# Performance work log

Measured on AMD Instinct MI355X. Metric: run time of the kernel, lower is better.

## Reference

```python
import jax, jax.numpy as jnp
import numpy as np

B, L, D, H, FF = 2, 2048, 2048, 16, 8192
DH = D // H
NEG = -1e9


def setup_inputs() -> dict:
    key = jax.random.key(0)
    ks = jax.random.split(key, 9)
    x = jax.random.normal(ks[0], (B, L, D), dtype=jnp.float32)
    # additive causal mask, broadcastable to [B, H, L, L]
    causal = jnp.triu(jnp.full((L, L), NEG, dtype=jnp.float32), k=1)
    mask = causal[None, None, :, :]
    s = 1.0 / np.sqrt(D)
    Wq = jax.random.normal(ks[1], (D, D), dtype=jnp.float32) * s
    Wk = jax.random.normal(ks[2], (D, D), dtype=jnp.float32) * s
    Wv = jax.random.normal(ks[3], (D, D), dtype=jnp.float32) * s
    Wo = jax.random.normal(ks[4], (D, D), dtype=jnp.float32) * s
    W_up = jax.random.normal(ks[5], (FF, D), dtype=jnp.float32) * s
    b_up = jnp.zeros((FF,), dtype=jnp.float32)
    W_down = jax.random.normal(ks[6], (D, FF), dtype=jnp.float32) * (1.0 / np.sqrt(FF))
    return {"x": x, "mask": mask, "Wq": Wq, "Wk": Wk, "Wv": Wv, "Wo": Wo,
            "W_up": W_up, "b_up": b_up, "W_down": W_down}


def reference(x, mask, Wq, Wk, Wv, Wo, W_up, b_up, W_down):
    b, l, d = x.shape
    # projections (torch Linear: y = x @ W.T); reshape to [B, H, L, DH]
    q = (x @ Wq.T).reshape(b, l, H, DH).transpose(0, 2, 1, 3)
    k = (x @ Wk.T).reshape(b, l, H, DH).transpose(0, 2, 1, 3)
    v = (x @ Wv.T).reshape(b, l, H, DH).transpose(0, 2, 1, 3)
    # NOTE: original module applies NO 1/sqrt(d_head) scaling
    scores = jnp.einsum('bhqd,bhkd->bhqk', q, k) + mask
    attn = jax.nn.softmax(scores, axis=-1)
    out = jnp.einsum('bhqk,bhkd->bhqd', attn, v)
    out = out.transpose(0, 2, 1, 3).reshape(b, l, d)
    x = x + out @ Wo.T
    h = jax.nn.relu(x @ W_up.T + b_up)
    return x + h @ W_down.T
```

## Files before the change

kernel.cpp:

```cpp
#include <hip/hip_runtime.h>
#include <stdint.h>

typedef _Float16 f16;
typedef __attribute__((ext_vector_type(8))) _Float16 f16x8;
typedef __attribute__((ext_vector_type(4))) _Float16 f16x4;
typedef __attribute__((ext_vector_type(4))) float f32x4;
typedef __attribute__((ext_vector_type(16))) float f32x16;

__device__ __forceinline__ void gload16(void* lds, const void* gc) {
  void* g = const_cast<void*>(gc);
  __builtin_amdgcn_global_load_lds((__attribute__((address_space(1))) void*)g,
                                   (__attribute__((address_space(3))) void*)lds,
                                   16, 0, 0);
}

__global__ __launch_bounds__(256) void k_cast(const float* __restrict__ in,
                                              f16* __restrict__ out, int n4) {
  int stride = gridDim.x * blockDim.x;
  for (int i = blockIdx.x * blockDim.x + threadIdx.x; i < n4; i += stride) {
    float4 v = ((const float4*)in)[i];
    f16x4 o;
    o[0] = (f16)v.x; o[1] = (f16)v.y; o[2] = (f16)v.z; o[3] = (f16)v.w;
    ((f16x4*)out)[i] = o;
  }
}

__global__ __launch_bounds__(256) void k_cast4(const float* __restrict__ s0, const float* __restrict__ s1,
                                               const float* __restrict__ s2, const float* __restrict__ s3,
                                               f16* __restrict__ d0, f16* __restrict__ d1,
                                               f16* __restrict__ d2, f16* __restrict__ d3, int n4) {
  const int which = blockIdx.y;
  const float* in = which == 0 ? s0 : which == 1 ? s1 : which == 2 ? s2 : s3;
  f16* out = which == 0 ? d0 : which == 1 ? d1 : which == 2 ? d2 : d3;
  int stride = gridDim.x * blockDim.x;
  for (int i = blockIdx.x * blockDim.x + threadIdx.x; i < n4; i += stride) {
    float4 v = ((const float4*)in)[i];
    f16x4 o;
    o[0] = (f16)v.x; o[1] = (f16)v.y; o[2] = (f16)v.z; o[3] = (f16)v.w;
    ((f16x4*)out)[i] = o;
  }
}

__global__ __launch_bounds__(256) void k_cast2w(const float* __restrict__ s0, const float* __restrict__ s1,
                                                f16* __restrict__ d0, f16* __restrict__ d1, int n4) {
  const int which = blockIdx.y;
  const float* in = which == 0 ? s0 : s1;
  f16* out = which == 0 ? d0 : d1;
  int stride = gridDim.x * blockDim.x;
  for (int i = blockIdx.x * blockDim.x + threadIdx.x; i < n4; i += stride) {
    float4 v = ((const float4*)in)[i];
    f16x4 o;
    o[0] = (f16)v.x; o[1] = (f16)v.y; o[2] = (f16)v.z; o[3] = (f16)v.w;
    ((f16x4*)out)[i] = o;
  }
}

__global__ __launch_bounds__(256) void k_transpose_v(const f16* __restrict__ vp,
                                                     f16* __restrict__ vt) {
  __shared__ __attribute__((aligned(16))) f16 tile[64][66];
  const int lt = blockIdx.x, dt = blockIdx.y, bh = blockIdx.z;
  const int t = threadIdx.x;
  const int r = t >> 3, c = 8 * (t & 7);
  const f16* src = vp + ((size_t)bh * 2048 + lt * 64) * 128 + dt * 64;
#pragma unroll
  for (int i = 0; i < 2; ++i) {
    union { f16x8 v; unsigned u[4]; } uu;
    uu.v = *(const f16x8*)&src[(size_t)(i * 32 + r) * 128 + c];
#pragma unroll
    for (int j = 0; j < 4; ++j)
      *(unsigned*)&tile[i * 32 + r][c + 2 * j] = uu.u[j];
  }
  __syncthreads();
  f16* dst = vt + ((size_t)bh * 128 + dt * 64) * 2048 + lt * 64;
#pragma unroll
  for (int i = 0; i < 2; ++i) {
    const int dr = i * 32 + r;
    f16x8 o;
#pragma unroll
    for (int e = 0; e < 8; ++e) o[e] = tile[c + e][dr];
    *(f16x8*)&dst[(size_t)dr * 2048 + c] = o;
  }
}

__global__ __launch_bounds__(256) void k_fuseout(const f16* __restrict__ x1b,
                                                 const float* __restrict__ p0,
                                                 const float* __restrict__ p1,
                                                 float* __restrict__ out, int n4) {
  int stride = gridDim.x * blockDim.x;
  for (int i = blockIdx.x * blockDim.x + threadIdx.x; i < n4; i += stride) {
    float4 a = ((const float4*)p0)[i];
    float4 b = ((const float4*)p1)[i];
    f16x4 xb = ((const f16x4*)x1b)[i];
    float4 o;
    o.x = (float)xb[0] + a.x + b.x;
    o.y = (float)xb[1] + a.y + b.y;
    o.z = (float)xb[2] + a.z + b.z;
    o.w = (float)xb[3] + a.w + b.w;
    ((float4*)out)[i] = o;
  }
}

template <int EPI, int SPLITOUT, int BK>
__global__ __launch_bounds__(256, 4) void gemm_nt(const f16* __restrict__ A,
                                                  const f16* __restrict__ B,
                                                  int Kit, int ld, int N,
                                                  const float* __restrict__ res,
                                                  const float* __restrict__ bias,
                                                  float* __restrict__ outf,
                                                  float* __restrict__ outf2,
                                                  f16* __restrict__ outb,
                                                  f16* __restrict__ outb_lo,
                                                  f16* __restrict__ outv) {
  constexpr int TSZ = 128 * BK;
  constexpr int CH  = 2048;
  constexpr int RPC = CH / BK;
  constexpr int NCH = 128 / RPC;
  constexpr int CW  = BK / 8;
  __shared__ __attribute__((aligned(16))) f16 As[TSZ];
  __shared__ __attribute__((aligned(16))) f16 Bs[TSZ];
  const int t = threadIdx.x;
  const int l = t & 63;
  const int w = t >> 6;
  const int wr = w >> 1, wc = w & 1;

  const int nwg = gridDim.x * gridDim.y;
  const int id = blockIdx.y * gridDim.x + blockIdx.x;
  const int sw = (id & 7) * (nwg >> 3) + (id >> 3);
  const int bn = sw % gridDim.x;
  const int bm = sw / gridDim.x;
  const int k0 = blockIdx.z * Kit;

  f32x4 acc[4][4] = {};

  const size_t aoff = (size_t)bm * 128 * ld + k0;
  const size_t boff = (size_t)bn * 128 * ld + k0;

  const int sr = t / CW;
  const int sc = 8 * (t % CW);
  const int lbase = w * 512;

  const int lr = l & 15, lq = l >> 4;
  const int nk = Kit / BK;
  for (int kt = 0; kt < nk; ++kt) {
    const size_t gbase = (size_t)kt * BK + (size_t)sr * ld + sc;
#pragma unroll
    for (int j = 0; j < NCH; ++j) {
      gload16(As + j * CH + lbase, A + aoff + (size_t)j * RPC * ld + gbase);
      gload16(Bs + j * CH + lbase, B + boff + (size_t)j * RPC * ld + gbase);
    }
    __syncthreads();
#pragma unroll
    for (int kk = 0; kk < BK / 32; ++kk) {
      f16x8 af[4], bfr[4];
#pragma unroll
      for (int m = 0; m < 4; ++m)
        af[m] = *(const f16x8*)&As[(wr * 64 + m * 16 + lr) * BK + kk * 32 + 8 * lq];
#pragma unroll
      for (int n = 0; n < 4; ++n)
        bfr[n] = *(const f16x8*)&Bs[(wc * 64 + n * 16 + lr) * BK + kk * 32 + 8 * lq];
#pragma unroll
      for (int m = 0; m < 4; ++m)
#pragma unroll
        for (int n = 0; n < 4; ++n)
          acc[m][n] = __builtin_amdgcn_mfma_f32_16x16x32_f16(af[m], bfr[n], acc[m][n], 0, 0, 0);
    }
    __syncthreads();
  }

  const size_t QKS = (size_t)8 << 20;
#pragma unroll
  for (int m = 0; m < 4; ++m) {
#pragma unroll
    for (int r = 0; r < 4; ++r) {
      const int grow = bm * 128 + wr * 64 + m * 16 + lq * 4 + r;
#pragma unroll
      for (int n = 0; n < 4; ++n) {
        const int gcol = bn * 128 + wc * 64 + n * 16 + lr;
        const float v = acc[m][n][r];
        if constexpr (EPI == 0) {
          const int which = gcol >> 11;
          const int hcol = gcol & 2047;
          const int bb = grow >> 11, ll = grow & 2047;
          const int hh = hcol >> 7, dh = hcol & 127;
          const size_t idx = ((size_t)((bb * 16 + hh) * 2048 + ll) << 7) + dh;
          const f16 hv = (f16)v;
          if (which == 2) {
            outv[idx] = hv;
          } else {
            outb[which * QKS + idx] = hv;
            if constexpr (SPLITOUT) outb_lo[which * QKS + idx] = (f16)(v - (float)hv);
          }
        } else if constexpr (EPI == 1) {
          const size_t idx = (size_t)grow * N + gcol;
          outb[idx] = (f16)(res[idx] + v);
        } else if constexpr (EPI == 2) {
          const size_t idx = (size_t)grow * N + gcol;
          outb[idx] = (f16)fmaxf(v + bias[gcol], 0.f);
        } else {
          const size_t idx = (size_t)grow * N + gcol;
          (blockIdx.z ? outf2 : outf)[idx] = v;
        }
      }
    }
  }
}

__global__ __launch_bounds__(256) void k_attn(const f16* __restrict__ q_hi,
                                              const f16* __restrict__ q_lo,
                                              const f16* __restrict__ k_hi,
                                              const f16* __restrict__ k_lo,
                                              const f16* __restrict__ vtp,
                                              f16* __restrict__ op) {
  __shared__ __attribute__((aligned(16))) f16 Ks_hi[64 * 128];
  __shared__ __attribute__((aligned(16))) f16 Ks_lo[64 * 128];
  __shared__ __attribute__((aligned(16))) f16 Vs[128 * 64];
  __shared__ __attribute__((aligned(16))) f16 Ps[4][32 * 64];
  const int t = threadIdx.x, l = t & 63, w = t >> 6;
  const int flat = (int)blockIdx.x;
  const int s_ = flat >> 5;
  const int bh = flat & 31;
  const int qb = (s_ < 8) ? (15 - s_) : (s_ - 8);
  const int q0 = qb * 128;
  const int lh = l >> 5, lm = l & 31;
  const int wrow0 = q0 + 32 * w;
  const int myrow = wrow0 + lm;

  const f16* qhp = q_hi + (size_t)bh * 2048 * 128;
  const f16* qlp = q_lo + (size_t)bh * 2048 * 128;
  const f16* khp = k_hi + (size_t)bh * 2048 * 128;
  const f16* klp = k_lo + (size_t)bh * 2048 * 128;
  const f16* vhp = vtp + (size_t)bh * 128 * 2048;

  const int krow = t >> 4, kg = t & 15;
  const int vrow = t >> 3, vg = t & 7;

  f16x8 aqh[8], aql[8];
#pragma unroll
  for (int c = 0; c < 8; ++c) {
    const size_t qi = (size_t)myrow * 128 + c * 16 + 8 * lh;
    aqh[c] = *(const f16x8*)&qhp[qi];
    aql[c] = *(const f16x8*)&qlp[qi];
  }

  f32x16 acc[4] = {};
  float mr[16], sr[16];
#pragma unroll
  for (int j = 0; j < 16; ++j) { mr[j] = -1e30f; sr[j] = 0.f; }

  const int ntile = 2 * qb + 2;
  for (int kt = 0; kt < ntile; ++kt) {
    f16x8 tkh[4], tkl[4], tv[4];
#pragma unroll
    for (int i = 0; i < 4; ++i) {
      const size_t ki = (size_t)(kt * 64 + i * 16 + krow) * 128 + 8 * kg;
      tkh[i] = *(const f16x8*)&khp[ki];
      tkl[i] = *(const f16x8*)&klp[ki];
      tv[i] = *(const f16x8*)&vhp[(size_t)(i * 32 + vrow) * 2048 + kt * 64 + 8 * vg];
    }
    __syncthreads();
#pragma unroll
    for (int i = 0; i < 4; ++i) {
      const int kr = i * 16 + krow;
      const int g = kg ^ (kr & 7);
      *(f16x8*)&Ks_hi[kr * 128 + 8 * g] = tkh[i];
      *(f16x8*)&Ks_lo[kr * 128 + 8 * g] = tkl[i];
      const int vr = i * 32 + vrow;
      const int gv = vg ^ (vr & 7);
      *(f16x8*)&Vs[vr * 64 + 8 * gv] = tv[i];
    }
    __syncthreads();

    if (kt * 64 >= wrow0 + 32) continue;

    f32x16 s0, s1;
    __builtin_amdgcn_s_setprio(1);
    {
      f32x16 zh = {}, zl = {};
#pragma unroll
      for (int c = 0; c < 8; ++c) {
        const int g = (2 * c + lh) ^ (lm & 7);
        const f16x8 bh_ = *(const f16x8*)&Ks_hi[lm * 128 + 8 * g];
        const f16x8 bl_ = *(const f16x8*)&Ks_lo[lm * 128 + 8 * g];
        zh = __builtin_amdgcn_mfma_f32_32x32x16_f16(aqh[c], bh_, zh, 0, 0, 0);
        zl = __builtin_amdgcn_mfma_f32_32x32x16_f16(aql[c], bh_, zl, 0, 0, 0);
        zl = __builtin_amdgcn_mfma_f32_32x32x16_f16(aqh[c], bl_, zl, 0, 0, 0);
      }
      s0 = zh + zl;
    }
    {
      f32x16 zh = {}, zl = {};
#pragma unroll
      for (int c = 0; c < 8; ++c) {
        const int g = (2 * c + lh) ^ (lm & 7);
        const f16x8 bh_ = *(const f16x8*)&Ks_hi[(32 + lm) * 128 + 8 * g];
        const f16x8 bl_ = *(const f16x8*)&Ks_lo[(32 + lm) * 128 + 8 * g];
        zh = __builtin_amdgcn_mfma_f32_32x32x16_f16(aqh[c], bh_, zh, 0, 0, 0);
        zl = __builtin_amdgcn_mfma_f32_32x32x16_f16(aql[c], bh_, zl, 0, 0, 0);
        zl = __builtin_amdgcn_mfma_f32_32x32x16_f16(aqh[c], bl_, zl, 0, 0, 0);
      }
      s1 = zh + zl;
    }
    __builtin_amdgcn_s_setprio(0);

    if (kt * 64 + 63 > wrow0) {
#pragma unroll
      for (int j = 0; j < 16; ++j) {
        const int rg = wrow0 + (j & 3) + 8 * (j >> 2) + 4 * lh;
        if (kt * 64 + lm > rg) s0[j] = -1e30f;
        if (kt * 64 + 32 + lm > rg) s1[j] = -1e30f;
      }
    }

    float mx[16];
#pragma unroll
    for (int j = 0; j < 16; ++j) {
      float m = fmaxf(s0[j], s1[j]);
#pragma unroll
      for (int off = 1; off < 32; off <<= 1)
        m = fmaxf(m, __shfl_xor(m, off));
      mx[j] = m;
    }
    bool grew = false;
#pragma unroll
    for (int j = 0; j < 16; ++j) grew = grew || (mx[j] > mr[j] + 8.f);
    if (__any(grew)) {
#pragma unroll
      for (int j = 0; j < 16; ++j) {
        const float mnew = fmaxf(mr[j], mx[j]);
        const float sc = __expf(mr[j] - mnew);
        mr[j] = mnew;
        sr[j] *= sc;
#pragma unroll
        for (int ct = 0; ct < 4; ++ct) acc[ct][j] *= sc;
      }
    }
#pragma unroll
    for (int j = 0; j < 16; ++j) {
      const int rjl = (j & 3) + 8 * (j >> 2) + 4 * lh;
      const float p0v = __expf(s0[j] - mr[j]);
      const float p1v = __expf(s1[j] - mr[j]);
      float ts = p0v + p1v;
#pragma unroll
      for (int off = 1; off < 32; off <<= 1)
        ts += __shfl_xor(ts, off);
      sr[j] += ts;
      const int g0 = (lm >> 3) ^ (rjl & 7);
      Ps[w][rjl * 64 + 8 * g0 + (lm & 7)] = (f16)p0v;
      const int g1 = (4 + (lm >> 3)) ^ (rjl & 7);
      Ps[w][rjl * 64 + 8 * g1 + (lm & 7)] = (f16)p1v;
    }

    f16x8 pf[4];
#pragma unroll
    for (int kk = 0; kk < 4; ++kk) {
      const int g = (2 * kk + lh) ^ (lm & 7);
      pf[kk] = *(const f16x8*)&Ps[w][lm * 64 + 8 * g];
    }
    __builtin_amdgcn_s_setprio(1);
#pragma unroll
    for (int ct = 0; ct < 4; ++ct) {
      const int dcol = ct * 32 + lm;
#pragma unroll
      for (int kk = 0; kk < 4; ++kk) {
        const int gv = (2 * kk + lh) ^ (dcol & 7);
        const f16x8 bv = *(const f16x8*)&Vs[dcol * 64 + 8 * gv];
        acc[ct] = __builtin_amdgcn_mfma_f32_32x32x16_f16(pf[kk], bv, acc[ct], 0, 0, 0);
      }
    }
    __builtin_amdgcn_s_setprio(0);
  }

  const int bb = bh >> 4, hh = bh & 15;
#pragma unroll
  for (int j = 0; j < 16; ++j) {
    const int rg = wrow0 + (j & 3) + 8 * (j >> 2) + 4 * lh;
    const float inv = 1.f / sr[j];
    const size_t row = (size_t)(bb * 2048 + rg);
#pragma unroll
    for (int ct = 0; ct < 4; ++ct)
      op[row * 2048 + hh * 128 + ct * 32 + lm] = (f16)(acc[ct][j] * inv);
  }
}

extern "C" void kernel_launch(void* const* d_in, const int* in_sizes, int n_in,
                              void* d_out, int out_size, void* d_ws, size_t ws_size,
                              hipStream_t stream) {
  const float* x   = (const float*)d_in[0];
  const float* Wq  = (const float*)d_in[2];
  const float* Wk  = (const float*)d_in[3];
  const float* Wv  = (const float*)d_in[4];
  const float* Wo  = (const float*)d_in[5];
  const float* Wup = (const float*)d_in[6];
  const float* bup = (const float*)d_in[7];
  const float* Wdn = (const float*)d_in[8];
  float* out = (float*)d_out;

  const size_t M1 = 1u << 20;
  f16* W = (f16*)d_ws;
  f16* x_hi    = W + 0 * M1;
  f16* wqkv_hi = W + 8 * M1;
  f16* wo_hi   = W + 20 * M1;
  f16* wup_hi  = W + 24 * M1;
  f16* wdn_hi  = W + 40 * M1;
  f16* q_hi    = W + 56 * M1;
  f16* q_lo    = W + 72 * M1;
  f16* vp      = W + 88 * M1;
  f16* vtb     = W + 96 * M1;
  f16* x1b   = x_hi;
  float* p0  = (float*)(W + 24 * M1);
  f16* hb    = W + 56 * M1;
  float* p1  = (float*)(W + 88 * M1);
  f16* attno = vp;
  if (ws_size < (size_t)104 * M1 * sizeof(f16)) return;

  auto cg = [](size_t n4) { size_t g = (n4 + 255) / 256; return (unsigned)(g > 2048 ? 2048 : g); };
  dim3 b256(256);
  k_cast<<<cg(2 * M1), b256, 0, stream>>>(x, x_hi, (int)(2 * M1));
  k_cast4<<<dim3(cg(1 * M1), 4), b256, 0, stream>>>(
      Wq, Wk, Wv, Wo,
      wqkv_hi, wqkv_hi + 4 * M1, wqkv_hi + 8 * M1, wo_hi, (int)(1 * M1));
  k_cast2w<<<dim3(cg(4 * M1), 2), b256, 0, stream>>>(
      Wup, Wdn, wup_hi, wdn_hi, (int)(4 * M1));

  gemm_nt<0, 1, 64><<<dim3(48, 32), b256, 0, stream>>>(
      x_hi, wqkv_hi, 2048, 2048, 6144,
      nullptr, nullptr, nullptr, nullptr, q_hi, q_lo, vp);
  k_transpose_v<<<dim3(32, 2, 32), b256, 0, stream>>>(vp, vtb);
  k_attn<<<dim3(512), b256, 0, stream>>>(
      q_hi, q_lo, q_hi + 8 * M1, q_lo + 8 * M1, vtb, attno);
  gemm_nt<1, 0, 64><<<dim3(16, 32), b256, 0, stream>>>(
      attno, wo_hi, 2048, 2048, 2048,
      x, nullptr, nullptr, nullptr, x1b, nullptr, nullptr);
  gemm_nt<2, 0, 64><<<dim3(64, 32), b256, 0, stream>>>(
      x1b, wup_hi, 2048, 2048, 8192,
      nullptr, bup, nullptr, nullptr, hb, nullptr, nullptr);
  gemm_nt<3, 0, 64><<<dim3(16, 32, 2), b256, 0, stream>>>(
      hb, wdn_hi, 4096, 8192, 2048,
      nullptr, nullptr, p0, p1, nullptr, nullptr, nullptr);
  k_fuseout<<<2048, b256, 0, stream>>>(x1b, p0, p1, out, (int)(2 * M1));
}
```

Baseline: 854.2 us.

## Compute transposed S tile so softmax stays in registers without LDS round-trip

Swaps the MFMA operand order so the score tile is transposed: each lane owns one query row. Row max and row sum then need only one cross-half shuffle instead of five-step butterflies per row, and the probabilities are packed to fp16 and redistributed through lane shuffles rather than written to and re-read from a shared-memory P buffer. Per-row rescale factors and the final normalisation are broadcast with shuffles. This cuts LDS traffic, shared-memory footprint and shuffle count, but adds more intricate register permutation logic and uses round-toward-zero packing.

```diff
diff --git a/kernel.cpp b/kernel.cpp
--- a/kernel.cpp
+++ b/kernel.cpp
@@ -4,14 +4,22 @@
 typedef _Float16 f16;
 typedef __attribute__((ext_vector_type(8))) _Float16 f16x8;
 typedef __attribute__((ext_vector_type(4))) _Float16 f16x4;
+typedef __attribute__((ext_vector_type(2))) __fp16 fp16x2;
 typedef __attribute__((ext_vector_type(4))) float f32x4;
 typedef __attribute__((ext_vector_type(16))) float f32x16;
+typedef __attribute__((ext_vector_type(4))) unsigned u32x4;
 
 __device__ __forceinline__ void gload16(void* lds, const void* gc) {
   void* g = const_cast<void*>(gc);
   __builtin_amdgcn_global_load_lds((__attribute__((address_space(1))) void*)g,
                                    (__attribute__((address_space(3))) void*)lds,
                                    16, 0, 0);
+}
+
+__device__ __forceinline__ unsigned pkrtz(float a, float b) {
+  union { fp16x2 h; unsigned u; } c;
+  c.h = __builtin_amdgcn_cvt_pkrtz(a, b);
+  return c.u;
 }
 
 __global__ __launch_bounds__(256) void k_cast(const float* __restrict__ in,
@@ -214,7 +222,6 @@
   __shared__ __attribute__((aligned(16))) f16 Ks_hi[64 * 128];
   __shared__ __attribute__((aligned(16))) f16 Ks_lo[64 * 128];
   __shared__ __attribute__((aligned(16))) f16 Vs[128 * 64];
-  __shared__ __attribute__((aligned(16))) f16 Ps[4][32 * 64];
   const int t = threadIdx.x, l = t & 63, w = t >> 6;
   const int flat = (int)blockIdx.x;
   const int s_ = flat >> 5;
@@ -243,9 +250,7 @@
   }
 
   f32x16 acc[4] = {};
-  float mr[16], sr[16];
-#pragma unroll
-  for (int j = 0; j < 16; ++j) { mr[j] = -1e30f; sr[j] = 0.f; }
+  float mr = -1e30f, sr = 0.f;
 
   const int ntile = 2 * qb + 2;
   for (int kt = 0; kt < ntile; ++kt) {
@@ -281,9 +286,9 @@
         const int g = (2 * c + lh) ^ (lm & 7);
         const f16x8 bh_ = *(const f16x8*)&Ks_hi[lm * 128 + 8 * g];
         const f16x8 bl_ = *(const f16x8*)&Ks_lo[lm * 128 + 8 * g];
-        zh = __builtin_amdgcn_mfma_f32_32x32x16_f16(aqh[c], bh_, zh, 0, 0, 0);
-        zl = __builtin_amdgcn_mfma_f32_32x32x16_f16(aql[c], bh_, zl, 0, 0, 0);
-        zl = __builtin_amdgcn_mfma_f32_32x32x16_f16(aqh[c], bl_, zl, 0, 0, 0);
+        zh = __builtin_amdgcn_mfma_f32_32x32x16_f16(bh_, aqh[c], zh, 0, 0, 0);
+        zl = __builtin_amdgcn_mfma_f32_32x32x16_f16(bh_, aql[c], zl, 0, 0, 0);
+        zl = __builtin_amdgcn_mfma_f32_32x32x16_f16(bl_, aqh[c], zl, 0, 0, 0);
       }
       s0 = zh + zl;
     }
@@ -294,9 +299,9 @@
         const int g = (2 * c + lh) ^ (lm & 7);
         const f16x8 bh_ = *(const f16x8*)&Ks_hi[(32 + lm) * 128 + 8 * g];
         const f16x8 bl_ = *(const f16x8*)&Ks_lo[(32 + lm) * 128 + 8 * g];
-        zh = __builtin_amdgcn_mfma_f32_32x32x16_f16(aqh[c], bh_, zh, 0, 0, 0);
-        zl = __builtin_amdgcn_mfma_f32_32x32x16_f16(aql[c], bh_, zl, 0, 0, 0);
-        zl = __builtin_amdgcn_mfma_f32_32x32x16_f16(aqh[c], bl_, zl, 0, 0, 0);
+        zh = __builtin_amdgcn_mfma_f32_32x32x16_f16(bh_, aqh[c], zh, 0, 0, 0);
+        zl = __builtin_amdgcn_mfma_f32_32x32x16_f16(bh_, aql[c], zl, 0, 0, 0);
+        zl = __builtin_amdgcn_mfma_f32_32x32x16_f16(bl_, aqh[c], zl, 0, 0, 0);
       }
       s1 = zh + zl;
     }
@@ -305,57 +310,65 @@
     if (kt * 64 + 63 > wrow0) {
 #pragma unroll
       for (int j = 0; j < 16; ++j) {
-        const int rg = wrow0 + (j & 3) + 8 * (j >> 2) + 4 * lh;
-        if (kt * 64 + lm > rg) s0[j] = -1e30f;
-        if (kt * 64 + 32 + lm > rg) s1[j] = -1e30f;
-      }
-    }
-
-    float mx[16];
+        const int keyl = (j & 3) + 8 * (j >> 2) + 4 * lh;
+        if (kt * 64 + keyl > myrow) s0[j] = -1e30f;
+        if (kt * 64 + 32 + keyl > myrow) s1[j] = -1e30f;
+      }
+    }
+
+    float m = -1e30f;
+#pragma unroll
+    for (int j = 0; j < 16; ++j) m = fmaxf(m, fmaxf(s0[j], s1[j]));
+    m = fmaxf(m, __shfl_xor(m, 32));
+    if (__any(m > mr + 8.f)) {
+      const float mnew = fmaxf(mr, m);
+      const float sc = __expf(mr - mnew);
+      mr = mnew;
+      sr *= sc;
+#pragma unroll
+      for (int j = 0; j < 16; ++j) {
+        const float scj = __shfl(sc, (j & 3) + 8 * (j >> 2) + 4 * lh + 32 * (l >> 5 ? 0 : 0));
+#pragma unroll
+        for (int ct = 0; ct < 4; ++ct) acc[ct][j] *= scj;
+      }
+    }
+    float p0v[16], p1v[16];
+    float ts = 0.f;
 #pragma unroll
     for (int j = 0; j < 16; ++j) {
-      float m = fmaxf(s0[j], s1[j]);
-#pragma unroll
-      for (int off = 1; off < 32; off <<= 1)
-        m = fmaxf(m, __shfl_xor(m, off));
-      mx[j] = m;
-    }
-    bool grew = false;
-#pragma unroll
-    for (int j = 0; j < 16; ++j) grew = grew || (mx[j] > mr[j] + 8.f);
-    if (__any(grew)) {
-#pragma unroll
-      for (int j = 0; j < 16; ++j) {
-        const float mnew = fmaxf(mr[j], mx[j]);
-        const float sc = __expf(mr[j] - mnew);
-        mr[j] = mnew;
-        sr[j] *= sc;
-#pragma unroll
-        for (int ct = 0; ct < 4; ++ct) acc[ct][j] *= sc;
-      }
-    }
-#pragma unroll
-    for (int j = 0; j < 16; ++j) {
-      const int rjl = (j & 3) + 8 * (j >> 2) + 4 * lh;
-      const float p0v = __expf(s0[j] - mr[j]);
-      const float p1v = __expf(s1[j] - mr[j]);
-      float ts = p0v + p1v;
-#pragma unroll
-      for (int off = 1; off < 32; off <<= 1)
-        ts += __shfl_xor(ts, off);
-      sr[j] += ts;
-      const int g0 = (lm >> 3) ^ (rjl & 7);
-      Ps[w][rjl * 64 + 8 * g0 + (lm & 7)] = (f16)p0v;
-      const int g1 = (4 + (lm >> 3)) ^ (rjl & 7);
-      Ps[w][rjl * 64 + 8 * g1 + (lm & 7)] = (f16)p1v;
-    }
-
+      p0v[j] = __expf(s0[j] - mr);
+      p1v[j] = __expf(s1[j] - mr);
+      ts += p0v[j] + p1v[j];
+    }
+    sr += ts + __shfl_xor(ts, 32);
+
+    unsigned u[16];
+#pragma unroll
+    for (int m2 = 0; m2 < 8; ++m2) {
+      u[m2] = pkrtz(p0v[2 * m2], p0v[2 * m2 + 1]);
+      u[8 + m2] = pkrtz(p1v[2 * m2], p1v[2 * m2 + 1]);
+    }
+    unsigned ys[8];
+#pragma unroll
+    for (int m2 = 0; m2 < 8; ++m2) {
+      const int q_ = m2 >> 1, h_ = m2 & 1;
+      const unsigned xs = lh ? u[4 * q_ + h_] : u[4 * q_ + 2 + h_];
+      ys[m2] = __shfl_xor(xs, 32);
+    }
     f16x8 pf[4];
 #pragma unroll
     for (int kk = 0; kk < 4; ++kk) {
-      const int g = (2 * kk + lh) ^ (lm & 7);
-      pf[kk] = *(const f16x8*)&Ps[w][lm * 64 + 8 * g];
-    }
+      union { u32x4 u4; f16x8 h8; } cv;
+      if (lh == 0) {
+        cv.u4[0] = u[4 * kk];     cv.u4[1] = u[4 * kk + 1];
+        cv.u4[2] = ys[2 * kk];    cv.u4[3] = ys[2 * kk + 1];
+      } else {
+        cv.u4[0] = ys[2 * kk];    cv.u4[1] = ys[2 * kk + 1];
+        cv.u4[2] = u[4 * kk + 2]; cv.u4[3] = u[4 * kk + 3];
+      }
+      pf[kk] = cv.h8;
+    }
+
     __builtin_amdgcn_s_setprio(1);
 #pragma unroll
     for (int ct = 0; ct < 4; ++ct) {
@@ -371,14 +384,15 @@
   }
 
   const int bb = bh >> 4, hh = bh & 15;
+  const float inv = 1.f / sr;
 #pragma unroll
   for (int j = 0; j < 16; ++j) {
-    const int rg = wrow0 + (j & 3) + 8 * (j >> 2) + 4 * lh;
-    const float inv = 1.f / sr[j];
-    const size_t row = (size_t)(bb * 2048 + rg);
+    const int rl = (j & 3) + 8 * (j >> 2) + 4 * lh;
+    const float invj = __shfl(inv, rl);
+    const size_t row = (size_t)(bb * 2048 + wrow0 + rl);
 #pragma unroll
     for (int ct = 0; ct < 4; ++ct)
-      op[row * 2048 + hh * 128 + ct * 32 + lm] = (f16)(acc[ct][j] * inv);
+      op[row * 2048 + hh * 128 + ct * 32 + lm] = (f16)(acc[ct][j] * invj);
   }
 }
 
```

Measured after the change: 752.7 us. -11.9%, faster.
